# Kernel optimization log

Measured on AMD Instinct MI355X. Metric: run time of the kernel, lower is better.

The kernel has to match this reference:

```python
import jax, jax.numpy as jnp
import numpy as np

B = 8192  # number of covariance matrices
N = 64    # n_assets


def setup_inputs() -> dict:
    key = jax.random.key(0)
    A = jax.random.normal(key, (B, N, N), dtype=jnp.float32)
    # SPD covariance: A A^T / N + 0.1 I  (real covariances are SPD)
    sigma = jnp.einsum('bij,bkj->bik', A, A) / N + 0.1 * jnp.eye(N, dtype=jnp.float32)
    return {"sigma": sigma}


def reference(sigma) -> jnp.ndarray:
    # Symmetrize, as the original does: 0.5 * (S + S^T)
    sym = 0.5 * (sigma + jnp.swapaxes(sigma, -1, -2))  # [B, N, N]
    n = sym.shape[-1]
    ones = jnp.ones((*sym.shape[:-2], n), dtype=sym.dtype)  # [B, N]
    # Closed-form min-variance (short selling allowed): w = S^-1 1 / (1^T S^-1 1)
    z = jnp.linalg.solve(sym, ones[..., None])[..., 0]      # [B, N]
    w = z / jnp.sum(z, axis=-1, keepdims=True)              # [B, N]
    return w[..., None]  # [B, N, 1], matching expand_dims(axis=-1)
```

## Files before the change

kernel.cpp:

```cpp
#include <hip/hip_runtime.h>


#define NN 64

typedef float v2f __attribute__((ext_vector_type(2)));
typedef float v4f __attribute__((ext_vector_type(4)));

template <int I> struct ic { static constexpr int value = I; };

template <int Start, int End, typename F>
__device__ __forceinline__ void static_for(F&& f) {
    if constexpr (Start < End) {
        f(ic<Start>{});
        static_for<Start + 1, End>(static_cast<F&&>(f));
    }
}

__device__ __forceinline__ float rlane(float v, int lane) {
    return __int_as_float(__builtin_amdgcn_readlane(__float_as_int(v), lane));
}

__device__ __forceinline__ float frcp(float x) {
#if __has_builtin(__builtin_amdgcn_rcpf)
    return __builtin_amdgcn_rcpf(x);
#else
    return 1.0f / x;
#endif
}

__global__
__attribute__((amdgpu_flat_work_group_size(256, 256), amdgpu_waves_per_eu(3, 3)))
void minvar_kernel(const float* __restrict__ sigma,
                   float* __restrict__ out,
                   int batch) {
    const int lane = threadIdx.x & 63;
    const int wid  = threadIdx.x >> 6;
    const int bid  = blockIdx.x * 4 + wid;
    if (bid >= batch) return;

    const float* __restrict__ p = sigma + (size_t)bid * (NN * NN) + (size_t)lane * NN;

    v2f r[NN / 2];
    static_for<0, NN / 4>([&](auto j4c) {
        constexpr int j4 = decltype(j4c)::value;
        v4f v = reinterpret_cast<const v4f*>(p)[j4];
        r[2 * j4 + 0] = v2f{v.x, v.y};
        r[2 * j4 + 1] = v2f{v.z, v.w};
    });

    float b = 1.0f;
    float d = 1.0f;

    static_for<0, 16>([&](auto pc) {
        constexpr int P  = decltype(pc)::value;
        constexpr int k0 = 4 * P;
        constexpr int m0 = 2 * P;

        const float el0  = r[m0].x;
        const float piv0 = rlane(el0, k0);
        const float nf0  = (lane != k0) ? (-el0 * frcp(piv0)) : 0.0f;
        d = (lane == k0) ? el0 : d;
        b = fmaf(nf0, rlane(b, k0), b);
        const float u01 = rlane(r[m0].y,     k0);
        const float u02 = rlane(r[m0 + 1].x, k0);
        const float u03 = rlane(r[m0 + 1].y, k0);
        r[m0].y     = fmaf(nf0, u01, r[m0].y);
        r[m0 + 1].x = fmaf(nf0, u02, r[m0 + 1].x);
        r[m0 + 1].y = fmaf(nf0, u03, r[m0 + 1].y);

        const float el1  = r[m0].y;
        const float piv1 = rlane(el1, k0 + 1);
        const float nf1  = (lane != k0 + 1) ? (-el1 * frcp(piv1)) : 0.0f;
        d = (lane == k0 + 1) ? el1 : d;
        b = fmaf(nf1, rlane(b, k0 + 1), b);
        const float u12 = rlane(r[m0 + 1].x, k0 + 1);
        const float u13 = rlane(r[m0 + 1].y, k0 + 1);
        r[m0 + 1].x = fmaf(nf1, u12, r[m0 + 1].x);
        r[m0 + 1].y = fmaf(nf1, u13, r[m0 + 1].y);

        const float el2  = r[m0 + 1].x;
        const float piv2 = rlane(el2, k0 + 2);
        const float nf2  = (lane != k0 + 2) ? (-el2 * frcp(piv2)) : 0.0f;
        d = (lane == k0 + 2) ? el2 : d;
        b = fmaf(nf2, rlane(b, k0 + 2), b);
        const float u23 = rlane(r[m0 + 1].y, k0 + 2);
        r[m0 + 1].y = fmaf(nf2, u23, r[m0 + 1].y);

        const float el3  = r[m0 + 1].y;
        const float piv3 = rlane(el3, k0 + 3);
        const float nf3  = (lane != k0 + 3) ? (-el3 * frcp(piv3)) : 0.0f;
        d = (lane == k0 + 3) ? el3 : d;
        b = fmaf(nf3, rlane(b, k0 + 3), b);

        if constexpr (P < 15) {
            static_for<m0 + 2, NN / 2>([&](auto mc) {
                constexpr int m  = decltype(mc)::value;
                constexpr int j0 = 2 * m;
                constexpr int j1 = 2 * m + 1;
                float ax = r[m].x, ay = r[m].y;
                ax = fmaf(nf0, rlane(el0, j0), ax);
                ay = fmaf(nf0, rlane(el0, j1), ay);
                ax = fmaf(nf1, rlane(el1, j0), ax);
                ay = fmaf(nf1, rlane(el1, j1), ay);
                ax = fmaf(nf2, rlane(el2, j0), ax);
                ay = fmaf(nf2, rlane(el2, j1), ay);
                ax = fmaf(nf3, rlane(el3, j0), ax);
                ay = fmaf(nf3, rlane(el3, j1), ay);
                r[m] = v2f{ax, ay};
            });
        }
    });

    const float z = b * frcp(d);

    float tot = z;
    #pragma unroll
    for (int off = 32; off >= 1; off >>= 1)
        tot += __shfl_xor(tot, off, 64);

    out[(size_t)bid * NN + lane] = z * frcp(tot);
}

extern "C" void kernel_launch(void* const* d_in, const int* in_sizes, int n_in,
                              void* d_out, int out_size, void* d_ws, size_t ws_size,
                              hipStream_t stream) {
    const float* sigma = (const float*)d_in[0];
    float* out = (float*)d_out;
    const int batch  = in_sizes[0] / (NN * NN);
    const int blocks = (batch + 3) / 4;
    minvar_kernel<<<blocks, 256, 0, stream>>>(sigma, out, batch);
}
```

Baseline: 216.4 us.

## Split each matrix's Gauss-Jordan elimination across two waves via shared memory

```diff
diff --git a/kernel.cpp b/kernel.cpp
--- a/kernel.cpp
+++ b/kernel.cpp
@@ -16,8 +16,8 @@
     }
 }
 
-__device__ __forceinline__ float rlane(float v, int lane) {
-    return __int_as_float(__builtin_amdgcn_readlane(__float_as_int(v), lane));
+__device__ __forceinline__ float rlane(float v, int l) {
+    return __int_as_float(__builtin_amdgcn_readlane(__float_as_int(v), l));
 }
 
 __device__ __forceinline__ float frcp(float x) {
@@ -29,96 +29,110 @@
 }
 
 __global__
-__attribute__((amdgpu_flat_work_group_size(256, 256), amdgpu_waves_per_eu(3, 3)))
+__attribute__((amdgpu_flat_work_group_size(128, 128), amdgpu_waves_per_eu(4, 6)))
 void minvar_kernel(const float* __restrict__ sigma,
                    float* __restrict__ out,
                    int batch) {
+    __shared__ float nfb[2][4][NN];
+    __shared__ float elb[2][4][NN];
+    __shared__ float zb[NN];
+
     const int lane = threadIdx.x & 63;
-    const int wid  = threadIdx.x >> 6;
-    const int bid  = blockIdx.x * 4 + wid;
+    const int w    = threadIdx.x >> 6;
+    const int bid  = blockIdx.x;
     if (bid >= batch) return;
 
     const float* __restrict__ p = sigma + (size_t)bid * (NN * NN) + (size_t)lane * NN;
 
-    v2f r[NN / 2];
-    static_for<0, NN / 4>([&](auto j4c) {
-        constexpr int j4 = decltype(j4c)::value;
-        v4f v = reinterpret_cast<const v4f*>(p)[j4];
-        r[2 * j4 + 0] = v2f{v.x, v.y};
-        r[2 * j4 + 1] = v2f{v.z, v.w};
-    });
+    v2f r[16];
+    auto load_half = [&](auto Wc) {
+        constexpr int W = decltype(Wc)::value;
+        static_for<0, 8>([&](auto gc) {
+            constexpr int g = decltype(gc)::value;
+            const v4f v = *reinterpret_cast<const v4f*>(p + 4 * (2 * g + W));
+            r[2 * g]     = v2f{v.x, v.y};
+            r[2 * g + 1] = v2f{v.z, v.w};
+        });
+    };
+    if (w == 0) load_half(ic<0>{}); else load_half(ic<1>{});
 
     float b = 1.0f;
     float d = 1.0f;
 
     static_for<0, 16>([&](auto pc) {
-        constexpr int P  = decltype(pc)::value;
-        constexpr int k0 = 4 * P;
-        constexpr int m0 = 2 * P;
+        constexpr int P     = decltype(pc)::value;
+        constexpr int owner = P & 1;
+        constexpr int k0    = 4 * P;
+        constexpr int m0    = 2 * (P >> 1);
 
-        const float el0  = r[m0].x;
-        const float piv0 = rlane(el0, k0);
-        const float nf0  = (lane != k0) ? (-el0 * frcp(piv0)) : 0.0f;
-        d = (lane == k0) ? el0 : d;
-        b = fmaf(nf0, rlane(b, k0), b);
-        const float u01 = rlane(r[m0].y,     k0);
-        const float u02 = rlane(r[m0 + 1].x, k0);
-        const float u03 = rlane(r[m0 + 1].y, k0);
-        r[m0].y     = fmaf(nf0, u01, r[m0].y);
-        r[m0 + 1].x = fmaf(nf0, u02, r[m0 + 1].x);
-        r[m0 + 1].y = fmaf(nf0, u03, r[m0 + 1].y);
+        float el[4], nf[4];
 
-        const float el1  = r[m0].y;
-        const float piv1 = rlane(el1, k0 + 1);
-        const float nf1  = (lane != k0 + 1) ? (-el1 * frcp(piv1)) : 0.0f;
-        d = (lane == k0 + 1) ? el1 : d;
-        b = fmaf(nf1, rlane(b, k0 + 1), b);
-        const float u12 = rlane(r[m0 + 1].x, k0 + 1);
-        const float u13 = rlane(r[m0 + 1].y, k0 + 1);
-        r[m0 + 1].x = fmaf(nf1, u12, r[m0 + 1].x);
-        r[m0 + 1].y = fmaf(nf1, u13, r[m0 + 1].y);
+        if (w == owner) {
+            static_for<0, 4>([&](auto cc) {
+                constexpr int c  = decltype(cc)::value;
+                constexpr int k  = k0 + c;
+                constexpr int mm = m0 + (c >> 1);
+                const float e = (c & 1) ? r[mm].y : r[mm].x;
+                elb[owner][c][lane] = e;
+                const float piv = rlane(e, k);
+                const float f   = (lane != k) ? (-e * frcp(piv)) : 0.0f;
+                nfb[owner][c][lane] = f;
+                d = (lane == k) ? e : d;
+                b = fmaf(f, rlane(b, k), b);
+                static_for<c + 1, 4>([&](auto jc) {
+                    constexpr int J  = decltype(jc)::value;
+                    constexpr int mj = m0 + (J >> 1);
+                    float v = (J & 1) ? r[mj].y : r[mj].x;
+                    v = fmaf(f, rlane(v, k), v);
+                    if constexpr (J & 1) r[mj].y = v; else r[mj].x = v;
+                });
+                el[c] = e; nf[c] = f;
+            });
+        }
+        __syncthreads();
+        if (w != owner) {
+            static_for<0, 4>([&](auto cc) {
+                constexpr int c = decltype(cc)::value;
+                nf[c] = nfb[owner][c][lane];
+                el[c] = elb[owner][c][lane];
+            });
+            static_for<0, 4>([&](auto cc) {
+                constexpr int c = decltype(cc)::value;
+                b = fmaf(nf[c], rlane(b, k0 + c), b);
+            });
+        }
 
-        const float el2  = r[m0 + 1].x;
-        const float piv2 = rlane(el2, k0 + 2);
-        const float nf2  = (lane != k0 + 2) ? (-el2 * frcp(piv2)) : 0.0f;
-        d = (lane == k0 + 2) ? el2 : d;
-        b = fmaf(nf2, rlane(b, k0 + 2), b);
-        const float u23 = rlane(r[m0 + 1].y, k0 + 2);
-        r[m0 + 1].y = fmaf(nf2, u23, r[m0 + 1].y);
-
-        const float el3  = r[m0 + 1].y;
-        const float piv3 = rlane(el3, k0 + 3);
-        const float nf3  = (lane != k0 + 3) ? (-el3 * frcp(piv3)) : 0.0f;
-        d = (lane == k0 + 3) ? el3 : d;
-        b = fmaf(nf3, rlane(b, k0 + 3), b);
-
-        if constexpr (P < 15) {
-            static_for<m0 + 2, NN / 2>([&](auto mc) {
+        auto trail = [&](auto Wc, auto Sc) {
+            constexpr int W = decltype(Wc)::value;
+            constexpr int S = decltype(Sc)::value;
+            static_for<S, 16>([&](auto mc) {
                 constexpr int m  = decltype(mc)::value;
-                constexpr int j0 = 2 * m;
-                constexpr int j1 = 2 * m + 1;
+                constexpr int j0 = 4 * (2 * (m >> 1) + W) + 2 * (m & 1);
+                constexpr int j1 = j0 + 1;
                 float ax = r[m].x, ay = r[m].y;
-                ax = fmaf(nf0, rlane(el0, j0), ax);
-                ay = fmaf(nf0, rlane(el0, j1), ay);
-                ax = fmaf(nf1, rlane(el1, j0), ax);
-                ay = fmaf(nf1, rlane(el1, j1), ay);
-                ax = fmaf(nf2, rlane(el2, j0), ax);
-                ay = fmaf(nf2, rlane(el2, j1), ay);
-                ax = fmaf(nf3, rlane(el3, j0), ax);
-                ay = fmaf(nf3, rlane(el3, j1), ay);
+                static_for<0, 4>([&](auto cc) {
+                    constexpr int c = decltype(cc)::value;
+                    ax = fmaf(nf[c], rlane(el[c], j0), ax);
+                    ay = fmaf(nf[c], rlane(el[c], j1), ay);
+                });
                 r[m] = v2f{ax, ay};
             });
-        }
+        };
+        if (w == owner) trail(ic<owner>{}, ic<m0 + 2>{});
+        else            trail(ic<1 - owner>{}, ic<(P & 1) ? (m0 + 2) : m0>{});
     });
 
     const float z = b * frcp(d);
-
-    float tot = z;
-    #pragma unroll
-    for (int off = 32; off >= 1; off >>= 1)
-        tot += __shfl_xor(tot, off, 64);
-
-    out[(size_t)bid * NN + lane] = z * frcp(tot);
+    if (((lane >> 2) & 1) == w) zb[lane] = z;
+    __syncthreads();
+    if (w == 0) {
+        const float zi = zb[lane];
+        float tot = zi;
+        #pragma unroll
+        for (int off = 32; off >= 1; off >>= 1)
+            tot += __shfl_xor(tot, off, 64);
+        out[(size_t)bid * NN + lane] = zi * frcp(tot);
+    }
 }
 
 extern "C" void kernel_launch(void* const* d_in, const int* in_sizes, int n_in,
@@ -126,7 +140,6 @@
                               hipStream_t stream) {
     const float* sigma = (const float*)d_in[0];
     float* out = (float*)d_out;
-    const int batch  = in_sizes[0] / (NN * NN);
-    const int blocks = (batch + 3) / 4;
-    minvar_kernel<<<blocks, 256, 0, stream>>>(sigma, out, batch);
+    const int batch = in_sizes[0] / (NN * NN);
+    minvar_kernel<<<batch, 128, 0, stream>>>(sigma, out, batch);
 }
```

After: 208.0 us. 3.9% less time.
